# Kernel optimization log

Hardware: AMD Instinct MI355X
Metric: run time of the kernel (lower is better)

## Reference

```python
import jax, jax.numpy as jnp
import numpy as np

B, L, M, H = 8, 256, 128, 768


def setup_inputs() -> dict:
    key = jax.random.key(0)
    ks = jax.random.split(key, 12)
    s = 1.0 / np.sqrt(H)
    sa = 1.0 / np.sqrt(2 * H)
    return {
        "text_features": jax.random.normal(ks[0], (B, L, H), jnp.float32),
        "dns_features": jax.random.normal(ks[1], (B, M, H), jnp.float32),
        # block 1 params (text_linear_1 has bias, dns_linear_1 no bias, att_linear_1: 2H->1)
        "W_t1": jax.random.uniform(ks[2], (H, H), jnp.float32, -s, s),
        "b_t1": jax.random.uniform(ks[3], (H,), jnp.float32, -s, s),
        "W_d1": jax.random.uniform(ks[4], (H, H), jnp.float32, -s, s),
        "w_att1": jax.random.uniform(ks[5], (2 * H,), jnp.float32, -sa, sa),
        "b_att1": jax.random.uniform(ks[6], (), jnp.float32, -sa, sa),
        # block 2 params (dns_linear_2 has bias, text_linear_2 no bias, att_linear_2: 2H->1)
        "W_d2": jax.random.uniform(ks[7], (H, H), jnp.float32, -s, s),
        "b_d2": jax.random.uniform(ks[8], (H,), jnp.float32, -s, s),
        "W_t2": jax.random.uniform(ks[9], (H, H), jnp.float32, -s, s),
        "w_att2": jax.random.uniform(ks[10], (2 * H,), jnp.float32, -sa, sa),
        "b_att2": jax.random.uniform(ks[11], (), jnp.float32, -sa, sa),
    }


def reference(text_features, dns_features, W_t1, b_t1, W_d1, w_att1, b_att1,
              W_d2, b_d2, W_t2, w_att2, b_att2):
    # Block 1: additive co-attention text -> dns.
    # tanh(cat([Lin(text_rep), Lin(dns_rep)])) @ w_att1 decomposes because tanh is
    # elementwise on the concat and the 2H->1 linear splits into two H-dot-products.
    t1 = jnp.tanh(jnp.einsum('blh,oh->blo', text_features, W_t1) + b_t1)  # (B,L,H)
    d1 = jnp.tanh(jnp.einsum('bmh,oh->bmo', dns_features, W_d1))          # (B,M,H)
    wa, wb = w_att1[:H], w_att1[H:]
    score1 = (t1 @ wa)[:, :, None] + (d1 @ wb)[:, None, :] + b_att1       # (B,L,M)
    a1 = jax.nn.softmax(score1, axis=-1)
    att_dns = jnp.einsum('blm,bmh->blh', a1, dns_features)                # (B,L,H)

    # Block 2: additive co-attention dns-context -> text.
    d2 = jnp.tanh(jnp.einsum('blh,oh->blo', att_dns, W_d2) + b_d2)        # (B,L,H)
    t2 = jnp.tanh(jnp.einsum('bjh,oh->bjo', text_features, W_t2))         # (B,L,H)
    wc, wd = w_att2[:H], w_att2[H:]
    score2 = (d2 @ wc)[:, :, None] + (t2 @ wd)[:, None, :] + b_att2       # (B,L,L)
    a2 = jax.nn.softmax(score2, axis=-1)
    att_text = jnp.einsum('blj,bjh->blh', a2, text_features)              # (B,L,H)

    return (att_text, att_dns)
```

## Files before the change

### kernel.cpp

```cpp
#include <hip/hip_runtime.h>
#include <hip/hip_bf16.h>
#include <math.h>

#define HH 768
#define NB 8
#define LL 256
#define MM 128
#define NROW1 (NB*MM)
#define NROW2 (NB*LL)
#define NROWS (NROW1+NROW2)
#define NCB 12

typedef __attribute__((ext_vector_type(8))) short  bf16x8;
typedef __attribute__((ext_vector_type(4))) float  f32x4;

static __device__ __forceinline__ unsigned int pkbf2(float a, float b) {
    __hip_bfloat162 h = __float22bfloat162_rn(make_float2(a, b));
    unsigned int u; __builtin_memcpy(&u, &h, 4); return u;
}

static __device__ __forceinline__ float fast_tanh(float x) {
    float e = __expf(2.0f * x);
    return 1.0f - 2.0f * __builtin_amdgcn_rcpf(e + 1.0f);
}

__global__ __launch_bounds__(256) void prep_bf16(
    const float4* __restrict__ text, const float4* __restrict__ dns,
    const float4* __restrict__ Wd1, const float4* __restrict__ Wt2,
    uint2* __restrict__ Xb, uint2* __restrict__ Wb)
{
    const int i = blockIdx.x * 256 + threadIdx.x;
    const float4* src; uint2* dst;
    if (i < 589824) {
        dst = Xb + i;
        src = (i < 196608) ? (dns + i) : (text + (i - 196608));
    } else {
        dst = Wb + (i - 589824);
        src = (i < 737280) ? (Wd1 + (i - 589824)) : (Wt2 + (i - 737280));
    }
    float4 v = *src;
    uint2 o; o.x = pkbf2(v.x, v.y); o.y = pkbf2(v.z, v.w);
    *dst = o;
}

__global__ __launch_bounds__(256) void score_mfma(
    const unsigned short* __restrict__ Xb, const unsigned short* __restrict__ Wb,
    const float* __restrict__ wv1, const float* __restrict__ wv2,
    float* __restrict__ partial)
{
    __shared__ __align__(16) unsigned short As[64][72];
    __shared__ __align__(16) unsigned short Bs[64][72];

    const int t = threadIdx.x;
    const int tile = (blockIdx.x >> 3) + (blockIdx.x & 7) * 72;
    const int rb = tile / 12, cb = tile % 12;
    const int row0 = rb * 64, col0 = cb * 64;

    const unsigned short* X = Xb + (size_t)row0 * HH;
    const unsigned short* W; const float* wv;
    if (row0 < NROW1) { W = Wb;                    wv = wv1; }
    else              { W = Wb + (size_t)HH * HH;  wv = wv2; }

    const int sr = t >> 2;
    const int c4 = t & 3;
    const unsigned short* xp = X + (size_t)sr * HH + c4 * 16;
    const unsigned short* wp = W + (size_t)(col0 + sr) * HH + c4 * 16;

    const int l  = t & 63;
    const int w  = t >> 6;
    const int wr = w * 16;
    const int lc = l & 15;
    const int lk = (l >> 4) * 8;

    f32x4 acc[4] = {};
    uint4 rA0, rA1, rB0, rB1, nA0, nA1, nB0, nB1;

    auto STAGE = [&]() {
        *reinterpret_cast<uint4*>(&As[sr][c4 * 16    ]) = rA0;
        *reinterpret_cast<uint4*>(&As[sr][c4 * 16 + 8]) = rA1;
        *reinterpret_cast<uint4*>(&Bs[sr][c4 * 16    ]) = rB0;
        *reinterpret_cast<uint4*>(&Bs[sr][c4 * 16 + 8]) = rB1;
    };
    auto MFMA_TILE = [&]() {
        #pragma unroll
        for (int kk = 0; kk < 2; ++kk) {
            const int ko = kk * 32 + lk;
            bf16x8 a = *reinterpret_cast<const bf16x8*>(&As[wr + lc][ko]);
            #pragma unroll
            for (int n = 0; n < 4; ++n) {
                bf16x8 b = *reinterpret_cast<const bf16x8*>(&Bs[n*16 + lc][ko]);
                acc[n] = __builtin_amdgcn_mfma_f32_16x16x32_bf16(a, b, acc[n], 0, 0, 0);
            }
        }
    };

    rA0 = *(const uint4*)(xp);     rA1 = *(const uint4*)(xp + 8);
    rB0 = *(const uint4*)(wp);     rB1 = *(const uint4*)(wp + 8);

    #pragma unroll 1
    for (int k0 = 0; k0 < HH - 64; k0 += 64) {
        STAGE();
        __syncthreads();
        nA0 = *(const uint4*)(xp + k0 + 64);  nA1 = *(const uint4*)(xp + k0 + 72);
        nB0 = *(const uint4*)(wp + k0 + 64);  nB1 = *(const uint4*)(wp + k0 + 72);
        MFMA_TILE();
        __syncthreads();
        rA0 = nA0; rA1 = nA1; rB0 = nB0; rB1 = nB1;
    }
    STAGE();
    __syncthreads();
    MFMA_TILE();

    float wvn[4];
    #pragma unroll
    for (int n = 0; n < 4; ++n) wvn[n] = wv[col0 + n*16 + lc];
    #pragma unroll
    for (int i = 0; i < 4; ++i) {
        float s = 0.f;
        #pragma unroll
        for (int n = 0; n < 4; ++n) s += fast_tanh(acc[n][i]) * wvn[n];
        s += __shfl_xor(s, 1);
        s += __shfl_xor(s, 2);
        s += __shfl_xor(s, 4);
        s += __shfl_xor(s, 8);
        if (lc == 0)
            partial[(size_t)(row0 + wr + (l >> 4)*4 + i) * NCB + cb] = s;
    }
}

__global__ __launch_bounds__(256) void tail_kernel(
    const float* __restrict__ text, const float* __restrict__ dns,
    const float* __restrict__ partial, float* __restrict__ out)
{
    const int b = blockIdx.x, hc = blockIdx.y;
    const int t = threadIdx.x;
    __shared__ float p1s[128], p2s[256], red[8];
    __shared__ __align__(16) float bt[256], bd[256];

    if (t < 128) {
        const float* pr = partial + (size_t)(b * MM + t) * NCB;
        float s = 0.f;
        #pragma unroll
        for (int c = 0; c < NCB; ++c) s += pr[c];
        p1s[t] = s;
    }
    {
        const float* pr = partial + (size_t)(NROW1 + b * LL + t) * NCB;
        float s = 0.f;
        #pragma unroll
        for (int c = 0; c < NCB; ++c) s += pr[c];
        p2s[t] = s;
    }
    __syncthreads();

    float x1 = (t < 128) ? p1s[t] : -1e30f;
    float m1 = x1;
    #pragma unroll
    for (int d = 1; d < 64; d <<= 1) m1 = fmaxf(m1, __shfl_xor(m1, d));
    if ((t & 63) == 0) red[t >> 6] = m1;
    float x2 = p2s[t];
    float m2 = x2;
    #pragma unroll
    for (int d = 1; d < 64; d <<= 1) m2 = fmaxf(m2, __shfl_xor(m2, d));
    if ((t & 63) == 0) red[4 + (t >> 6)] = m2;
    __syncthreads();
    m1 = fmaxf(fmaxf(red[0], red[1]), fmaxf(red[2], red[3]));
    m2 = fmaxf(fmaxf(red[4], red[5]), fmaxf(red[6], red[7]));

    float e1 = (t < 128) ? __expf(x1 - m1) : 0.f;
    float e2 = __expf(x2 - m2);
    __syncthreads();
    float s1 = e1, s2 = e2;
    #pragma unroll
    for (int d = 1; d < 64; d <<= 1) { s1 += __shfl_xor(s1, d); s2 += __shfl_xor(s2, d); }
    if ((t & 63) == 0) { red[t >> 6] = s1; red[4 + (t >> 6)] = s2; }
    __syncthreads();
    s1 = red[0] + red[1] + red[2] + red[3];
    s2 = red[4] + red[5] + red[6] + red[7];
    if (t < 128) p1s[t] = e1 / s1;
    p2s[t] = e2 / s2;
    __syncthreads();

    const int hh  = hc * 16 + (t & 15);
    const int rsl = t >> 4;

    const int jr0 = rsl * 16;
    float st = 0.f;
    #pragma unroll
    for (int r = 0; r < 16; ++r)
        st = fmaf(p2s[jr0 + r], text[(size_t)(b * LL + jr0 + r) * HH + hh], st);

    const int mr0 = rsl * 8;
    float sd = 0.f;
    #pragma unroll
    for (int r = 0; r < 8; ++r)
        sd = fmaf(p1s[mr0 + r], dns[(size_t)(b * MM + mr0 + r) * HH + hh], sd);

    bt[t] = st; bd[t] = sd;
    __syncthreads();
    if (t < 128) { bt[t] += bt[t + 128]; bd[t] += bd[t + 128]; } __syncthreads();
    if (t < 64)  { bt[t] += bt[t + 64];  bd[t] += bd[t + 64];  } __syncthreads();
    if (t < 32)  { bt[t] += bt[t + 32];  bd[t] += bd[t + 32];  } __syncthreads();
    if (t < 16)  { bt[t] += bt[t + 16];  bd[t] += bd[t + 16];  }
    __syncthreads();

    const int H4 = HH / 4;
    const int n4out = NB * LL * H4;
    const float4* svt4 = reinterpret_cast<const float4*>(bt);
    const float4* svd4 = reinterpret_cast<const float4*>(bd);
    float4* out4 = reinterpret_cast<float4*>(out);
    #pragma unroll
    for (int i = t; i < LL * 4; i += 256) {
        const int ll = i >> 2, c4 = i & 3;
        const size_t o = (size_t)(b * LL + ll) * H4 + hc * 4 + c4;
        out4[o] = svt4[c4];
        out4[n4out + o] = svd4[c4];
    }
}

extern "C" void kernel_launch(void* const* d_in, const int* in_sizes, int n_in,
                              void* d_out, int out_size, void* d_ws, size_t ws_size,
                              hipStream_t stream) {
    const float* text   = (const float*)d_in[0];
    const float* dns    = (const float*)d_in[1];
    const float* W_d1   = (const float*)d_in[4];
    const float* w_att1 = (const float*)d_in[5];
    const float* W_t2   = (const float*)d_in[9];
    const float* w_att2 = (const float*)d_in[10];

    float* ws      = (float*)d_ws;
    float* partial = ws;
    unsigned short* Xb = (unsigned short*)(ws + 36864);
    unsigned short* Wb = Xb + (size_t)NROWS * HH;
    float* out     = (float*)d_out;

    prep_bf16<<<3456, 256, 0, stream>>>(
        (const float4*)text, (const float4*)dns, (const float4*)W_d1,
        (const float4*)W_t2, (uint2*)Xb, (uint2*)Wb);
    score_mfma<<<576, 256, 0, stream>>>(
        Xb, Wb, w_att1 + HH, w_att2 + HH, partial);
    tail_kernel<<<dim3(NB, 48), 256, 0, stream>>>(text, dns, partial, out);
}
```

Before: 30.71 us.

## Load A fragments directly to registers and double-buffer B tiles in LDS

The GEMM-score kernel no longer stages the activation tile through shared memory. Each lane now loads its MFMA A fragment straight from global memory into registers. The weight tile is double-buffered in LDS with a two-deep register prefetch, which cuts the syncs per K-step from two to one. This removes LDS traffic and a barrier but makes the global A loads less coalesced, since each lane reads 16-byte chunks scattered across rows.

```diff
diff --git a/kernel.cpp b/kernel.cpp
--- a/kernel.cpp
+++ b/kernel.cpp
@@ -48,8 +48,7 @@
     const float* __restrict__ wv1, const float* __restrict__ wv2,
     float* __restrict__ partial)
 {
-    __shared__ __align__(16) unsigned short As[64][72];
-    __shared__ __align__(16) unsigned short Bs[64][72];
+    __shared__ __align__(16) unsigned short Bs[2][64][72];
 
     const int t = threadIdx.x;
     const int tile = (blockIdx.x >> 3) + (blockIdx.x & 7) * 72;
@@ -63,7 +62,6 @@
 
     const int sr = t >> 2;
     const int c4 = t & 3;
-    const unsigned short* xp = X + (size_t)sr * HH + c4 * 16;
     const unsigned short* wp = W + (size_t)(col0 + sr) * HH + c4 * 16;
 
     const int l  = t & 63;
@@ -72,44 +70,53 @@
     const int lc = l & 15;
     const int lk = (l >> 4) * 8;
 
+    const unsigned short* ap = X + (size_t)(wr + lc) * HH + lk;
+
     f32x4 acc[4] = {};
-    uint4 rA0, rA1, rB0, rB1, nA0, nA1, nB0, nB1;
-
-    auto STAGE = [&]() {
-        *reinterpret_cast<uint4*>(&As[sr][c4 * 16    ]) = rA0;
-        *reinterpret_cast<uint4*>(&As[sr][c4 * 16 + 8]) = rA1;
-        *reinterpret_cast<uint4*>(&Bs[sr][c4 * 16    ]) = rB0;
-        *reinterpret_cast<uint4*>(&Bs[sr][c4 * 16 + 8]) = rB1;
-    };
-    auto MFMA_TILE = [&]() {
+    uint4 rB0, rB1, rA0, rA1, nA0, nA1;
+
+    rB0 = *(const uint4*)(wp);
+    rB1 = *(const uint4*)(wp + 8);
+    *reinterpret_cast<uint4*>(&Bs[0][sr][c4 * 16    ]) = rB0;
+    *reinterpret_cast<uint4*>(&Bs[0][sr][c4 * 16 + 8]) = rB1;
+    rB0 = *(const uint4*)(wp + 64);
+    rB1 = *(const uint4*)(wp + 72);
+    rA0 = *(const uint4*)(ap);
+    rA1 = *(const uint4*)(ap + 32);
+    __syncthreads();
+
+    #pragma unroll 1
+    for (int k0 = 0; k0 < HH; k0 += 64) {
+        const int cur = (k0 >> 6) & 1;
+        const bool more = (k0 + 64 < HH);
+
+        if (more) {
+            nA0 = *(const uint4*)(ap + k0 + 64);
+            nA1 = *(const uint4*)(ap + k0 + 96);
+        }
+
         #pragma unroll
         for (int kk = 0; kk < 2; ++kk) {
             const int ko = kk * 32 + lk;
-            bf16x8 a = *reinterpret_cast<const bf16x8*>(&As[wr + lc][ko]);
+            bf16x8 a = (kk == 0) ? *(const bf16x8*)&rA0 : *(const bf16x8*)&rA1;
             #pragma unroll
             for (int n = 0; n < 4; ++n) {
-                bf16x8 b = *reinterpret_cast<const bf16x8*>(&Bs[n*16 + lc][ko]);
+                bf16x8 b = *reinterpret_cast<const bf16x8*>(&Bs[cur][n*16 + lc][ko]);
                 acc[n] = __builtin_amdgcn_mfma_f32_16x16x32_bf16(a, b, acc[n], 0, 0, 0);
             }
         }
-    };
-
-    rA0 = *(const uint4*)(xp);     rA1 = *(const uint4*)(xp + 8);
-    rB0 = *(const uint4*)(wp);     rB1 = *(const uint4*)(wp + 8);
-
-    #pragma unroll 1
-    for (int k0 = 0; k0 < HH - 64; k0 += 64) {
-        STAGE();
-        __syncthreads();
-        nA0 = *(const uint4*)(xp + k0 + 64);  nA1 = *(const uint4*)(xp + k0 + 72);
-        nB0 = *(const uint4*)(wp + k0 + 64);  nB1 = *(const uint4*)(wp + k0 + 72);
-        MFMA_TILE();
-        __syncthreads();
-        rA0 = nA0; rA1 = nA1; rB0 = nB0; rB1 = nB1;
-    }
-    STAGE();
-    __syncthreads();
-    MFMA_TILE();
+
+        if (more) {
+            *reinterpret_cast<uint4*>(&Bs[cur ^ 1][sr][c4 * 16    ]) = rB0;
+            *reinterpret_cast<uint4*>(&Bs[cur ^ 1][sr][c4 * 16 + 8]) = rB1;
+            if (k0 + 128 < HH) {
+                rB0 = *(const uint4*)(wp + k0 + 128);
+                rB1 = *(const uint4*)(wp + k0 + 136);
+            }
+            __syncthreads();
+            rA0 = nA0; rA1 = nA1;
+        }
+    }
 
     float wvn[4];
     #pragma unroll
```

New measurement: 31.68 us. 1.03x slower.

## Fuse bf16 conversion into score GEMM and load A fragments directly from global

Applied to the files above, without the earlier changes.

Removes the separate prep kernel that converted activations and weights to bf16 in workspace. The GEMM now reads fp32 inputs directly, converting B tiles to bf16 before staging them in shared memory. A fragments are loaded straight from global into registers in MFMA layout, so the A shared-memory tile goes away. This saves a kernel launch and a full write/read pass over the bf16 copies, at the cost of twice the global read bytes per tile, more registers, and A loads that are less coalesced.

```diff
diff --git a/kernel.cpp b/kernel.cpp
--- a/kernel.cpp
+++ b/kernel.cpp
@@ -24,31 +24,12 @@
     return 1.0f - 2.0f * __builtin_amdgcn_rcpf(e + 1.0f);
 }
 
-__global__ __launch_bounds__(256) void prep_bf16(
-    const float4* __restrict__ text, const float4* __restrict__ dns,
-    const float4* __restrict__ Wd1, const float4* __restrict__ Wt2,
-    uint2* __restrict__ Xb, uint2* __restrict__ Wb)
-{
-    const int i = blockIdx.x * 256 + threadIdx.x;
-    const float4* src; uint2* dst;
-    if (i < 589824) {
-        dst = Xb + i;
-        src = (i < 196608) ? (dns + i) : (text + (i - 196608));
-    } else {
-        dst = Wb + (i - 589824);
-        src = (i < 737280) ? (Wd1 + (i - 589824)) : (Wt2 + (i - 737280));
-    }
-    float4 v = *src;
-    uint2 o; o.x = pkbf2(v.x, v.y); o.y = pkbf2(v.z, v.w);
-    *dst = o;
-}
-
-__global__ __launch_bounds__(256) void score_mfma(
-    const unsigned short* __restrict__ Xb, const unsigned short* __restrict__ Wb,
+__global__ __launch_bounds__(256) void score_fused(
+    const float* __restrict__ text, const float* __restrict__ dns,
+    const float* __restrict__ Wd1, const float* __restrict__ Wt2,
     const float* __restrict__ wv1, const float* __restrict__ wv2,
     float* __restrict__ partial)
 {
-    __shared__ __align__(16) unsigned short As[64][72];
     __shared__ __align__(16) unsigned short Bs[64][72];
 
     const int t = threadIdx.x;
@@ -56,15 +37,13 @@
     const int rb = tile / 12, cb = tile % 12;
     const int row0 = rb * 64, col0 = cb * 64;
 
-    const unsigned short* X = Xb + (size_t)row0 * HH;
-    const unsigned short* W; const float* wv;
-    if (row0 < NROW1) { W = Wb;                    wv = wv1; }
-    else              { W = Wb + (size_t)HH * HH;  wv = wv2; }
+    const float* Xsrc; const float* W; const float* wv; int rbase;
+    if (row0 < NROW1) { Xsrc = dns;  rbase = row0;         W = Wd1; wv = wv1; }
+    else              { Xsrc = text; rbase = row0 - NROW1; W = Wt2; wv = wv2; }
 
     const int sr = t >> 2;
     const int c4 = t & 3;
-    const unsigned short* xp = X + (size_t)sr * HH + c4 * 16;
-    const unsigned short* wp = W + (size_t)(col0 + sr) * HH + c4 * 16;
+    const float* wp = W + (size_t)(col0 + sr) * HH + c4 * 16;
 
     const int l  = t & 63;
     const int w  = t >> 6;
@@ -72,20 +51,40 @@
     const int lc = l & 15;
     const int lk = (l >> 4) * 8;
 
+    const float* ap = Xsrc + (size_t)(rbase + wr + lc) * HH + lk;
+
     f32x4 acc[4] = {};
-    uint4 rA0, rA1, rB0, rB1, nA0, nA1, nB0, nB1;
-
-    auto STAGE = [&]() {
-        *reinterpret_cast<uint4*>(&As[sr][c4 * 16    ]) = rA0;
-        *reinterpret_cast<uint4*>(&As[sr][c4 * 16 + 8]) = rA1;
-        *reinterpret_cast<uint4*>(&Bs[sr][c4 * 16    ]) = rB0;
-        *reinterpret_cast<uint4*>(&Bs[sr][c4 * 16 + 8]) = rB1;
+    float4 rB[4], nB[4], rA[4], nA[4];
+
+    auto STAGE_B = [&]() {
+        uint4 p0, p1;
+        p0.x = pkbf2(rB[0].x, rB[0].y); p0.y = pkbf2(rB[0].z, rB[0].w);
+        p0.z = pkbf2(rB[1].x, rB[1].y); p0.w = pkbf2(rB[1].z, rB[1].w);
+        p1.x = pkbf2(rB[2].x, rB[2].y); p1.y = pkbf2(rB[2].z, rB[2].w);
+        p1.z = pkbf2(rB[3].x, rB[3].y); p1.w = pkbf2(rB[3].z, rB[3].w);
+        *reinterpret_cast<uint4*>(&Bs[sr][c4 * 16    ]) = p0;
+        *reinterpret_cast<uint4*>(&Bs[sr][c4 * 16 + 8]) = p1;
+    };
+    auto LOAD_B = [&](float4 (&r)[4], int k0) {
+        #pragma unroll
+        for (int q = 0; q < 4; ++q) r[q] = *(const float4*)(wp + k0 + q * 4);
+    };
+    auto LOAD_A = [&](float4 (&r)[4], int k0) {
+        r[0] = *(const float4*)(ap + k0);
+        r[1] = *(const float4*)(ap + k0 + 4);
+        r[2] = *(const float4*)(ap + k0 + 32);
+        r[3] = *(const float4*)(ap + k0 + 36);
     };
     auto MFMA_TILE = [&]() {
         #pragma unroll
         for (int kk = 0; kk < 2; ++kk) {
+            uint4 af;
+            af.x = pkbf2(rA[2*kk].x,   rA[2*kk].y);
+            af.y = pkbf2(rA[2*kk].z,   rA[2*kk].w);
+            af.z = pkbf2(rA[2*kk+1].x, rA[2*kk+1].y);
+            af.w = pkbf2(rA[2*kk+1].z, rA[2*kk+1].w);
+            bf16x8 a = *reinterpret_cast<const bf16x8*>(&af);
             const int ko = kk * 32 + lk;
-            bf16x8 a = *reinterpret_cast<const bf16x8*>(&As[wr + lc][ko]);
             #pragma unroll
             for (int n = 0; n < 4; ++n) {
                 bf16x8 b = *reinterpret_cast<const bf16x8*>(&Bs[n*16 + lc][ko]);
@@ -94,20 +93,21 @@
         }
     };
 
-    rA0 = *(const uint4*)(xp);     rA1 = *(const uint4*)(xp + 8);
-    rB0 = *(const uint4*)(wp);     rB1 = *(const uint4*)(wp + 8);
+    LOAD_B(rB, 0);
+    LOAD_A(rA, 0);
 
     #pragma unroll 1
     for (int k0 = 0; k0 < HH - 64; k0 += 64) {
-        STAGE();
+        STAGE_B();
         __syncthreads();
-        nA0 = *(const uint4*)(xp + k0 + 64);  nA1 = *(const uint4*)(xp + k0 + 72);
-        nB0 = *(const uint4*)(wp + k0 + 64);  nB1 = *(const uint4*)(wp + k0 + 72);
+        LOAD_B(nB, k0 + 64);
+        LOAD_A(nA, k0 + 64);
         MFMA_TILE();
         __syncthreads();
-        rA0 = nA0; rA1 = nA1; rB0 = nB0; rB1 = nB1;
-    }
-    STAGE();
+        #pragma unroll
+        for (int q = 0; q < 4; ++q) { rB[q] = nB[q]; rA[q] = nA[q]; }
+    }
+    STAGE_B();
     __syncthreads();
     MFMA_TILE();
 
@@ -230,14 +230,9 @@
 
     float* ws      = (float*)d_ws;
     float* partial = ws;
-    unsigned short* Xb = (unsigned short*)(ws + 36864);
-    unsigned short* Wb = Xb + (size_t)NROWS * HH;
     float* out     = (float*)d_out;
 
-    prep_bf16<<<3456, 256, 0, stream>>>(
-        (const float4*)text, (const float4*)dns, (const float4*)W_d1,
-        (const float4*)W_t2, (uint2*)Xb, (uint2*)Wb);
-    score_mfma<<<576, 256, 0, stream>>>(
-        Xb, Wb, w_att1 + HH, w_att2 + HH, partial);
+    score_fused<<<576, 256, 0, stream>>>(
+        text, dns, W_d1, W_t2, w_att1 + HH, w_att2 + HH, partial);
     tail_kernel<<<dim3(NB, 48), 256, 0, stream>>>(text, dns, partial, out);
 }
```

Result: slower. 40.49 us (+31.8%).

## Halve score GEMM tile width and load A fragments directly into registers

Applied to the files above, without the earlier changes.

The score GEMM tile narrows from 64x64 to 64x32 columns, which doubles the grid to 1152 blocks and the partial-sum column blocks to 24. The A operand is no longer staged through shared memory. Each lane loads its MFMA A fragment straight from global memory into registers, so only B goes through LDS. The aim is more parallelism across CUs, lower LDS traffic and less work per barrier, at the cost of more redundant global reads of X and twice as many partials for the tail kernel to reduce.

```diff
diff --git a/kernel.cpp b/kernel.cpp
--- a/kernel.cpp
+++ b/kernel.cpp
@@ -9,7 +9,7 @@
 #define NROW1 (NB*MM)
 #define NROW2 (NB*LL)
 #define NROWS (NROW1+NROW2)
-#define NCB 12
+#define NCB 24
 
 typedef __attribute__((ext_vector_type(8))) short  bf16x8;
 typedef __attribute__((ext_vector_type(4))) float  f32x4;
@@ -48,23 +48,21 @@
     const float* __restrict__ wv1, const float* __restrict__ wv2,
     float* __restrict__ partial)
 {
-    __shared__ __align__(16) unsigned short As[64][72];
-    __shared__ __align__(16) unsigned short Bs[64][72];
+    __shared__ __align__(16) unsigned short Bs[32][72];
 
     const int t = threadIdx.x;
-    const int tile = (blockIdx.x >> 3) + (blockIdx.x & 7) * 72;
-    const int rb = tile / 12, cb = tile % 12;
-    const int row0 = rb * 64, col0 = cb * 64;
+    const int tile = (blockIdx.x >> 3) + (blockIdx.x & 7) * 144;
+    const int rb = tile / NCB, cb = tile % NCB;
+    const int row0 = rb * 64, col0 = cb * 32;
 
     const unsigned short* X = Xb + (size_t)row0 * HH;
     const unsigned short* W; const float* wv;
     if (row0 < NROW1) { W = Wb;                    wv = wv1; }
     else              { W = Wb + (size_t)HH * HH;  wv = wv2; }
 
-    const int sr = t >> 2;
-    const int c4 = t & 3;
-    const unsigned short* xp = X + (size_t)sr * HH + c4 * 16;
-    const unsigned short* wp = W + (size_t)(col0 + sr) * HH + c4 * 16;
+    const int sr = t >> 3;
+    const int kc = (t & 7) * 8;
+    const unsigned short* wp = W + (size_t)(col0 + sr) * HH + kc;
 
     const int l  = t & 63;
     const int w  = t >> 6;
@@ -72,53 +70,49 @@
     const int lc = l & 15;
     const int lk = (l >> 4) * 8;
 
-    f32x4 acc[4] = {};
-    uint4 rA0, rA1, rB0, rB1, nA0, nA1, nB0, nB1;
-
-    auto STAGE = [&]() {
-        *reinterpret_cast<uint4*>(&As[sr][c4 * 16    ]) = rA0;
-        *reinterpret_cast<uint4*>(&As[sr][c4 * 16 + 8]) = rA1;
-        *reinterpret_cast<uint4*>(&Bs[sr][c4 * 16    ]) = rB0;
-        *reinterpret_cast<uint4*>(&Bs[sr][c4 * 16 + 8]) = rB1;
-    };
+    const unsigned short* ap = X + (size_t)(wr + lc) * HH + lk;
+
+    f32x4 acc[2] = {};
+    uint4 rB, nB, rA0, rA1, nA0, nA1;
+
+    rB  = *(const uint4*)(wp);
+    rA0 = *(const uint4*)(ap);
+    rA1 = *(const uint4*)(ap + 32);
+
     auto MFMA_TILE = [&]() {
         #pragma unroll
         for (int kk = 0; kk < 2; ++kk) {
             const int ko = kk * 32 + lk;
-            bf16x8 a = *reinterpret_cast<const bf16x8*>(&As[wr + lc][ko]);
+            bf16x8 a = (kk == 0) ? *(const bf16x8*)&rA0 : *(const bf16x8*)&rA1;
             #pragma unroll
-            for (int n = 0; n < 4; ++n) {
+            for (int n = 0; n < 2; ++n) {
                 bf16x8 b = *reinterpret_cast<const bf16x8*>(&Bs[n*16 + lc][ko]);
                 acc[n] = __builtin_amdgcn_mfma_f32_16x16x32_bf16(a, b, acc[n], 0, 0, 0);
             }
         }
     };
 
-    rA0 = *(const uint4*)(xp);     rA1 = *(const uint4*)(xp + 8);
-    rB0 = *(const uint4*)(wp);     rB1 = *(const uint4*)(wp + 8);
-
     #pragma unroll 1
     for (int k0 = 0; k0 < HH - 64; k0 += 64) {
-        STAGE();
+        *reinterpret_cast<uint4*>(&Bs[sr][kc]) = rB;
         __syncthreads();
-        nA0 = *(const uint4*)(xp + k0 + 64);  nA1 = *(const uint4*)(xp + k0 + 72);
-        nB0 = *(const uint4*)(wp + k0 + 64);  nB1 = *(const uint4*)(wp + k0 + 72);
+        nB  = *(const uint4*)(wp + k0 + 64);
+        nA0 = *(const uint4*)(ap + k0 + 64);
+        nA1 = *(const uint4*)(ap + k0 + 96);
         MFMA_TILE();
         __syncthreads();
-        rA0 = nA0; rA1 = nA1; rB0 = nB0; rB1 = nB1;
-    }
-    STAGE();
+        rB = nB; rA0 = nA0; rA1 = nA1;
+    }
+    *reinterpret_cast<uint4*>(&Bs[sr][kc]) = rB;
     __syncthreads();
     MFMA_TILE();
 
-    float wvn[4];
-    #pragma unroll
-    for (int n = 0; n < 4; ++n) wvn[n] = wv[col0 + n*16 + lc];
+    float wvn[2];
+    #pragma unroll
+    for (int n = 0; n < 2; ++n) wvn[n] = wv[col0 + n*16 + lc];
     #pragma unroll
     for (int i = 0; i < 4; ++i) {
-        float s = 0.f;
-        #pragma unroll
-        for (int n = 0; n < 4; ++n) s += fast_tanh(acc[n][i]) * wvn[n];
+        float s = fast_tanh(acc[0][i]) * wvn[0] + fast_tanh(acc[1][i]) * wvn[1];
         s += __shfl_xor(s, 1);
         s += __shfl_xor(s, 2);
         s += __shfl_xor(s, 4);
@@ -230,14 +224,14 @@
 
     float* ws      = (float*)d_ws;
     float* partial = ws;
-    unsigned short* Xb = (unsigned short*)(ws + 36864);
+    unsigned short* Xb = (unsigned short*)(ws + 73728);
     unsigned short* Wb = Xb + (size_t)NROWS * HH;
     float* out     = (float*)d_out;
 
     prep_bf16<<<3456, 256, 0, stream>>>(
         (const float4*)text, (const float4*)dns, (const float4*)W_d1,
         (const float4*)W_t2, (uint2*)Xb, (uint2*)Wb);
-    score_mfma<<<576, 256, 0, stream>>>(
+    score_mfma<<<1152, 256, 0, stream>>>(
         Xb, Wb, w_att1 + HH, w_att2 + HH, partial);
     tail_kernel<<<dim3(NB, 48), 256, 0, stream>>>(text, dns, partial, out);
 }
```

Result: slower. 36.72 us (+19.6%).
